# Kernel tuning notes

Hardware: AMD Instinct MI355X
Metric: run time of the kernel (lower is better)

The kernel has to match this reference:

```python
import jax, jax.numpy as jnp
import numpy as np

BETA = 0.25
ALPHA = 0.5
K = 1024
D = 64


def setup_inputs() -> dict:
    key = jax.random.key(0)
    k1, k2 = jax.random.split(key)
    latents = jax.random.normal(k1, (32, D, 64, 64), dtype=jnp.float32)  # NCHW
    # nn.Embedding init uniform_(-1/K, 1/K)
    emb_weight = jax.random.uniform(k2, (K, D), dtype=jnp.float32, minval=-1.0 / K, maxval=1.0 / K)
    return {"latents": latents, "emb_weight": emb_weight}


def reference(latents, emb_weight):
    # NCHW -> NHWC
    x = jnp.transpose(latents, (0, 2, 3, 1))  # [B,H,W,D]
    B, H, W, Dd = x.shape
    flat = x.reshape(-1, Dd)  # [N,D]

    dist = (jnp.sum(flat * flat, axis=1, keepdims=True)
            + jnp.sum(emb_weight * emb_weight, axis=1)
            - 2.0 * flat @ emb_weight.T)
    inds = jnp.argmin(dist, axis=1)  # [N]

    # one-hot @ W == gather
    q = emb_weight[inds].reshape(B, H, W, Dd)

    commitment_loss = jnp.mean((jax.lax.stop_gradient(q) - x) ** 2)
    embedding_loss = jnp.mean((q - jax.lax.stop_gradient(x)) ** 2)
    vq_loss = commitment_loss * BETA + embedding_loss * ALPHA

    alpha_q = 2.0 * ALPHA / (B * H * W * Dd)
    q_st = x + alpha_q * q + jax.lax.stop_gradient((1.0 - alpha_q) * q - x)

    out = jnp.transpose(q_st, (0, 3, 1, 2))  # NHWC -> NCHW
    return out, vq_loss, inds.reshape(B, H, W)
```

## Files before the change

kernel.cpp:

```cpp
#include <hip/hip_runtime.h>

typedef __attribute__((ext_vector_type(8))) short bf16x8;
typedef __attribute__((ext_vector_type(4))) float f32x4;
typedef __attribute__((ext_vector_type(4))) int   i32x4;

#define NROWS     131072
#define KCODES    1024
#define DDIM      64
#define OUT_ELEMS 8388608
#define NBLK      1024
#define MAGICF    12582912.0f
#define MARGIN    240
#define WS_PART   0
#define WS_SE     (8*1024)
#define WS_SEM    (12*1024)
#define WS_BPREP  (16*1024)

__device__ __forceinline__ float pairwise64_sq(const float* __restrict__ v) {
#pragma clang fp contract(off)
    float r[8];
#pragma unroll
    for (int j = 0; j < 8; ++j) r[j] = v[j] * v[j];
#pragma unroll
    for (int i = 8; i < 64; i += 8) {
#pragma unroll
        for (int j = 0; j < 8; ++j) r[j] += v[i + j] * v[i + j];
    }
    return ((r[0] + r[1]) + (r[2] + r[3])) + ((r[4] + r[5]) + (r[6] + r[7]));
}

__device__ __forceinline__ int med3i(int a, int b, int c) {
    int mn = min(a, b), mx = max(a, b);
    return max(mn, min(mx, c));
}

__device__ __forceinline__ unsigned short rne_bf16(float v) {
    unsigned u = __float_as_uint(v);
    return (unsigned short)((u + 0x7fffu + ((u >> 16) & 1u)) >> 16);
}

__global__ __launch_bounds__(256) void vq_prep(
    const float* __restrict__ emb, float* __restrict__ se,
    float* __restrict__ sem, unsigned short* __restrict__ bprep)
{
#pragma clang fp contract(off)
    const int k = blockIdx.x * 256 + threadIdx.x;
    if (k >= KCODES) return;
    const float* e = emb + (k << 6);
    float s = pairwise64_sq(e);
    se[k]  = s;
    sem[k] = (s * 65536.0f) + MAGICF;

    const int c = k >> 4, slot = k & 15;
#pragma unroll
    for (int f = 0; f < 2; ++f) {
#pragma unroll
        for (int g = 0; g < 4; ++g) {
            unsigned short h[8];
#pragma unroll
            for (int j = 0; j < 8; ++j)
                h[j] = rne_bf16(e[f * 32 + g * 8 + j] * 256.0f);
            int4 w;
            w.x = h[0] | (h[1] << 16); w.y = h[2] | (h[3] << 16);
            w.z = h[4] | (h[5] << 16); w.w = h[6] | (h[7] << 16);
            *reinterpret_cast<int4*>(bprep + (((c * 2 + f) * 64 + (g * 16 + slot)) << 3)) = w;
        }
    }
}

__global__ __launch_bounds__(256, 2) void vq_main(
    const float* __restrict__ lat, const float* __restrict__ emb,
    const float* __restrict__ se_g, const float* __restrict__ sem_g,
    const unsigned short* __restrict__ bprep,
    float* __restrict__ out, double* __restrict__ partials)
{
#pragma clang fp contract(off)
    __shared__ float  x_lds[128 * 67];
    __shared__ float  se_lds[KCODES];
    __shared__ float  sem_lds[KCODES];
    __shared__ int    keys_lds[128 * 49];
    __shared__ int    idx_lds[128];
    __shared__ double wsum[4];

    const int tid = threadIdx.x, l = tid & 63, wv = tid >> 6;
    const int blk = blockIdx.x;
    const int n0 = blk * 128, b = n0 >> 12, hw0 = n0 & 4095;

    {
        const int row = tid & 127, dh = (tid >> 7) * 32;
#pragma unroll
        for (int dd = 0; dd < 32; ++dd) {
            int d = dh + dd;
            x_lds[row * 67 + d] = lat[((size_t)b << 18) + ((size_t)d << 12) + hw0 + row];
        }
    }
    for (int i = tid; i < KCODES; i += 256) { se_lds[i] = se_g[i]; sem_lds[i] = sem_g[i]; }
    __syncthreads();

    bf16x8 afrag[2][2];
#pragma unroll
    for (int T = 0; T < 2; ++T) {
        const float* xr = x_lds + (wv * 32 + T * 16 + (l & 15)) * 67;
        const int kb = (l >> 4) << 3;
#pragma unroll
        for (int kh = 0; kh < 2; ++kh) {
            bf16x8 f;
#pragma unroll
            for (int j = 0; j < 8; ++j)
                f[j] = (short)rne_bf16(xr[kh * 32 + kb + j] * -512.0f);
            afrag[T][kh] = f;
        }
    }

    int m1[2][4], m2[2][4], m3[2][4];
#pragma unroll
    for (int T = 0; T < 2; ++T)
#pragma unroll
        for (int r = 0; r < 4; ++r) { m1[T][r] = m2[T][r] = m3[T][r] = 0x7fffffff; }

    const i32x4* bp = reinterpret_cast<const i32x4*>(bprep);
    i32x4 bbuf[2][2];
    bbuf[0][0] = bp[l];
    bbuf[0][1] = bp[64 + l];

#pragma unroll 2
    for (int c = 0; c < 64; ++c) {
        const int cur = c & 1, nxt = cur ^ 1;
        if (c < 63) {
            bbuf[nxt][0] = bp[(c + 1) * 128 + l];
            bbuf[nxt][1] = bp[(c + 1) * 128 + 64 + l];
        }
        const float sevm = sem_lds[c * 16 + (l & 15)];
        bf16x8 b0 = __builtin_bit_cast(bf16x8, bbuf[cur][0]);
        bf16x8 b1 = __builtin_bit_cast(bf16x8, bbuf[cur][1]);
        const unsigned code0 = (unsigned)((c << 4) + (l & 15));
#pragma unroll
        for (int T = 0; T < 2; ++T) {
            f32x4 acc = {0.f, 0.f, 0.f, 0.f};
            acc = __builtin_amdgcn_mfma_f32_16x16x32_bf16(afrag[T][0], b0, acc, 0, 0, 0);
            acc = __builtin_amdgcn_mfma_f32_16x16x32_bf16(afrag[T][1], b1, acc, 0, 0, 0);
#pragma unroll
            for (int r = 0; r < 4; ++r) {
                float uf = acc[r] + sevm;
                int key = (int)((__float_as_uint(uf) << 10) | code0);
                int n1 = min(key, m1[T][r]);
                int n2 = med3i(key, m1[T][r], m2[T][r]);
                int n3 = med3i(max(key, m1[T][r]), m2[T][r], m3[T][r]);
                m1[T][r] = n1; m2[T][r] = n2; m3[T][r] = n3;
            }
        }
    }

#pragma unroll
    for (int T = 0; T < 2; ++T) {
#pragma unroll
        for (int r = 0; r < 4; ++r) {
            const int rloc = wv * 32 + T * 16 + ((l >> 4) << 2) + r;
            keys_lds[rloc * 49 + (l & 15) * 3 + 0] = m1[T][r];
            keys_lds[rloc * 49 + (l & 15) * 3 + 1] = m2[T][r];
            keys_lds[rloc * 49 + (l & 15) * 3 + 2] = m3[T][r];
        }
    }
    __syncthreads();

    if (tid < 128) {
        const int row = tid;
        int mk = 0x7fffffff;
#pragma unroll 4
        for (int i = 0; i < 48; ++i) mk = min(mk, keys_lds[row * 49 + i]);
        const int lim = mk + (MARGIN << 10) + 1023;
        const float* xr = x_lds + row * 67;
        const float sx = pairwise64_sq(xr);
        float bestd = 3.4e38f; int besti = KCODES;
        for (int i = 0; i < 48; ++i) {
            int key = keys_lds[row * 49 + i];
            if (key <= lim) {
                int code = key & 1023;
                const float* e = emb + (code << 6);
                float g = 0.0f;
#pragma unroll
                for (int d = 0; d < 64; ++d) g = fmaf(xr[d], e[d], g);
                float s_   = sx + se_lds[code];
                float dist = s_ - 2.0f * g;
                if (dist < bestd || (dist == bestd && code < besti)) { bestd = dist; besti = code; }
            }
        }
        idx_lds[row] = besti;
    }
    __syncthreads();

    double lsum = 0.0;
    {
        const float aq = 1.0f / 8388608.0f;
        const int row = tid & 127, dh = (tid >> 7) * 32;
        const int code = idx_lds[row];
        float q[32];
        const float4* eq4 = reinterpret_cast<const float4*>(emb + (code << 6) + dh);
#pragma unroll
        for (int qq = 0; qq < 8; ++qq) {
            float4 v = eq4[qq];
            q[qq * 4 + 0] = v.x; q[qq * 4 + 1] = v.y; q[qq * 4 + 2] = v.z; q[qq * 4 + 3] = v.w;
        }
        float* ob = out + ((size_t)b << 18) + hw0 + row;
#pragma unroll
        for (int dd = 0; dd < 32; ++dd) {
            int d = dh + dd;
            float xv = x_lds[row * 67 + d];
            float qd = q[dd];
            float v  = (xv + aq * qd) + ((1.0f - aq) * qd - xv);
            ob[(size_t)d << 12] = v;
            float diff = qd - xv;
            lsum += (double)diff * (double)diff;
        }
    }
    if (tid < 128) out[OUT_ELEMS + 1 + (size_t)n0 + tid] = (float)idx_lds[tid];

#pragma unroll
    for (int off = 32; off > 0; off >>= 1) lsum += __shfl_down(lsum, off, 64);
    if (l == 0) wsum[wv] = lsum;
    __syncthreads();
    if (tid == 0) partials[blk] = (wsum[0] + wsum[1]) + (wsum[2] + wsum[3]);
}

__global__ __launch_bounds__(512) void vq_finish(
    const double* __restrict__ partials, float* __restrict__ out)
{
    __shared__ double lds[8];
    const int t = threadIdx.x;
    double s = partials[t] + partials[t + 512];
#pragma unroll
    for (int off = 32; off > 0; off >>= 1) s += __shfl_down(s, off, 64);
    if ((t & 63) == 0) lds[t >> 6] = s;
    __syncthreads();
    if (t == 0) {
        double tot = 0.0;
#pragma unroll
        for (int i = 0; i < 8; ++i) tot += lds[i];
        out[OUT_ELEMS] = (float)(0.75 * tot / (double)OUT_ELEMS);
    }
}

extern "C" void kernel_launch(void* const* d_in, const int* in_sizes, int n_in,
                              void* d_out, int out_size, void* d_ws, size_t ws_size,
                              hipStream_t stream)
{
    const float* lat = (const float*)d_in[0];
    const float* emb = (const float*)d_in[1];
    float* out = (float*)d_out;
    char* ws = (char*)d_ws;

    double* partials      = (double*)(ws + WS_PART);
    float* se             = (float*)(ws + WS_SE);
    float* sem            = (float*)(ws + WS_SEM);
    unsigned short* bprep = (unsigned short*)(ws + WS_BPREP);

    vq_prep<<<dim3(4),    dim3(256), 0, stream>>>(emb, se, sem, bprep);
    vq_main<<<dim3(NBLK), dim3(256), 0, stream>>>(lat, emb, se, sem, bprep, out, partials);
    vq_finish<<<dim3(1),  dim3(512), 0, stream>>>(partials, out);
}
```

Measured before the change: 97.60 us.

## Halve rows per block and split candidate rescoring across four lanes

Each block now handles 64 rows instead of 128, doubling the grid to 2048 blocks. Each wave now computes one 16-row MFMA tile instead of two. The exact-distance rescoring of the top-3 candidates, previously done serially by 128 threads over 48 keys, is now split across four lanes per row with shuffle reductions. This is meant to raise occupancy and balance the serial refinement phase, at the cost of loading the codebook prefetch and se tables twice as often per row. The change in x-norm summation order may slightly alter tie-breaking numerics.

```diff
diff --git a/kernel.cpp b/kernel.cpp
--- a/kernel.cpp
+++ b/kernel.cpp
@@ -6,15 +6,16 @@
 
 #define NROWS     131072
 #define KCODES    1024
-#define DDIM      64
 #define OUT_ELEMS 8388608
-#define NBLK      1024
+#define RPB       64
+#define NBLK      2048
 #define MAGICF    12582912.0f
 #define MARGIN    240
+#define XSTRIDE   67
 #define WS_PART   0
-#define WS_SE     (8*1024)
-#define WS_SEM    (12*1024)
-#define WS_BPREP  (16*1024)
+#define WS_SE     (16*1024)
+#define WS_SEM    (20*1024)
+#define WS_BPREP  (24*1024)
 
 __device__ __forceinline__ float pairwise64_sq(const float* __restrict__ v) {
 #pragma clang fp contract(off)
@@ -75,48 +76,46 @@
     float* __restrict__ out, double* __restrict__ partials)
 {
 #pragma clang fp contract(off)
-    __shared__ float  x_lds[128 * 67];
+    __shared__ float  x_lds[RPB * XSTRIDE];
     __shared__ float  se_lds[KCODES];
     __shared__ float  sem_lds[KCODES];
-    __shared__ int    keys_lds[128 * 49];
-    __shared__ int    idx_lds[128];
+    __shared__ int    keys_lds[RPB * 49];
+    __shared__ int    idx_lds[RPB];
     __shared__ double wsum[4];
 
     const int tid = threadIdx.x, l = tid & 63, wv = tid >> 6;
     const int blk = blockIdx.x;
-    const int n0 = blk * 128, b = n0 >> 12, hw0 = n0 & 4095;
-
-    {
-        const int row = tid & 127, dh = (tid >> 7) * 32;
-#pragma unroll
-        for (int dd = 0; dd < 32; ++dd) {
-            int d = dh + dd;
-            x_lds[row * 67 + d] = lat[((size_t)b << 18) + ((size_t)d << 12) + hw0 + row];
+    const int n0 = blk * RPB, b = n0 >> 12, hw0 = n0 & 4095;
+    const float* latb = lat + ((size_t)b << 18) + hw0;
+
+    {
+        const int row = tid & 63, dbase = (tid >> 6) * 16;
+#pragma unroll
+        for (int dd = 0; dd < 16; ++dd) {
+            int d = dbase + dd;
+            x_lds[row * XSTRIDE + d] = latb[((size_t)d << 12) + row];
         }
     }
     for (int i = tid; i < KCODES; i += 256) { se_lds[i] = se_g[i]; sem_lds[i] = sem_g[i]; }
     __syncthreads();
 
-    bf16x8 afrag[2][2];
-#pragma unroll
-    for (int T = 0; T < 2; ++T) {
-        const float* xr = x_lds + (wv * 32 + T * 16 + (l & 15)) * 67;
-        const int kb = (l >> 4) << 3;
+    bf16x8 afrag[2];
+    {
+        const int arow = l & 15, kb = (l >> 4) << 3;
+        const float* xr = x_lds + (wv * 16 + arow) * XSTRIDE;
 #pragma unroll
         for (int kh = 0; kh < 2; ++kh) {
             bf16x8 f;
 #pragma unroll
             for (int j = 0; j < 8; ++j)
                 f[j] = (short)rne_bf16(xr[kh * 32 + kb + j] * -512.0f);
-            afrag[T][kh] = f;
-        }
-    }
-
-    int m1[2][4], m2[2][4], m3[2][4];
-#pragma unroll
-    for (int T = 0; T < 2; ++T)
-#pragma unroll
-        for (int r = 0; r < 4; ++r) { m1[T][r] = m2[T][r] = m3[T][r] = 0x7fffffff; }
+            afrag[kh] = f;
+        }
+    }
+
+    int m1[4], m2[4], m3[4];
+#pragma unroll
+    for (int r = 0; r < 4; ++r) { m1[r] = m2[r] = m3[r] = 0x7fffffff; }
 
     const i32x4* bp = reinterpret_cast<const i32x4*>(bprep);
     i32x4 bbuf[2][2];
@@ -134,86 +133,105 @@
         bf16x8 b0 = __builtin_bit_cast(bf16x8, bbuf[cur][0]);
         bf16x8 b1 = __builtin_bit_cast(bf16x8, bbuf[cur][1]);
         const unsigned code0 = (unsigned)((c << 4) + (l & 15));
-#pragma unroll
-        for (int T = 0; T < 2; ++T) {
-            f32x4 acc = {0.f, 0.f, 0.f, 0.f};
-            acc = __builtin_amdgcn_mfma_f32_16x16x32_bf16(afrag[T][0], b0, acc, 0, 0, 0);
-            acc = __builtin_amdgcn_mfma_f32_16x16x32_bf16(afrag[T][1], b1, acc, 0, 0, 0);
-#pragma unroll
-            for (int r = 0; r < 4; ++r) {
-                float uf = acc[r] + sevm;
-                int key = (int)((__float_as_uint(uf) << 10) | code0);
-                int n1 = min(key, m1[T][r]);
-                int n2 = med3i(key, m1[T][r], m2[T][r]);
-                int n3 = med3i(max(key, m1[T][r]), m2[T][r], m3[T][r]);
-                m1[T][r] = n1; m2[T][r] = n2; m3[T][r] = n3;
-            }
-        }
-    }
-
-#pragma unroll
-    for (int T = 0; T < 2; ++T) {
+        f32x4 acc = {0.f, 0.f, 0.f, 0.f};
+        acc = __builtin_amdgcn_mfma_f32_16x16x32_bf16(afrag[0], b0, acc, 0, 0, 0);
+        acc = __builtin_amdgcn_mfma_f32_16x16x32_bf16(afrag[1], b1, acc, 0, 0, 0);
 #pragma unroll
         for (int r = 0; r < 4; ++r) {
-            const int rloc = wv * 32 + T * 16 + ((l >> 4) << 2) + r;
-            keys_lds[rloc * 49 + (l & 15) * 3 + 0] = m1[T][r];
-            keys_lds[rloc * 49 + (l & 15) * 3 + 1] = m2[T][r];
-            keys_lds[rloc * 49 + (l & 15) * 3 + 2] = m3[T][r];
-        }
-    }
-    __syncthreads();
-
-    if (tid < 128) {
-        const int row = tid;
+            float uf = acc[r] + sevm;
+            int key = (int)((__float_as_uint(uf) << 10) | code0);
+            int n1 = min(key, m1[r]);
+            int n2 = med3i(key, m1[r], m2[r]);
+            int n3 = med3i(max(key, m1[r]), m2[r], m3[r]);
+            m1[r] = n1; m2[r] = n2; m3[r] = n3;
+        }
+    }
+
+#pragma unroll
+    for (int r = 0; r < 4; ++r) {
+        const int rloc = wv * 16 + ((l >> 4) << 2) + r;
+        keys_lds[rloc * 49 + (l & 15) * 3 + 0] = m1[r];
+        keys_lds[rloc * 49 + (l & 15) * 3 + 1] = m2[r];
+        keys_lds[rloc * 49 + (l & 15) * 3 + 2] = m3[r];
+    }
+    __syncthreads();
+
+    {
+        const int row = tid >> 2, h = tid & 3;
+        const int kbase = row * 49 + h * 12;
         int mk = 0x7fffffff;
+#pragma unroll
+        for (int i = 0; i < 12; ++i) mk = min(mk, keys_lds[kbase + i]);
+        mk = min(mk, __shfl_xor(mk, 1, 64));
+        mk = min(mk, __shfl_xor(mk, 2, 64));
+        const int lim = mk + (MARGIN << 10) + 1023;
+
+        const float* xr = x_lds + row * XSTRIDE;
+        float rr0 = 0.0f, rr1 = 0.0f;
+#pragma unroll
+        for (int i = 0; i < 64; i += 8) {
+            float v0 = xr[i + 2 * h];
+            float v1 = xr[i + 2 * h + 1];
+            rr0 += v0 * v0;
+            rr1 += v1 * v1;
+        }
+        float s_h = rr0 + rr1;
+        float p   = s_h + __shfl_xor(s_h, 1, 64);
+        float sx  = p + __shfl_xor(p, 2, 64);
+
+        float bestd = 3.4e38f; int besti = KCODES;
 #pragma unroll 4
-        for (int i = 0; i < 48; ++i) mk = min(mk, keys_lds[row * 49 + i]);
-        const int lim = mk + (MARGIN << 10) + 1023;
-        const float* xr = x_lds + row * 67;
-        const float sx = pairwise64_sq(xr);
-        float bestd = 3.4e38f; int besti = KCODES;
-        for (int i = 0; i < 48; ++i) {
-            int key = keys_lds[row * 49 + i];
+        for (int i = 0; i < 12; ++i) {
+            int key = keys_lds[kbase + i];
             if (key <= lim) {
                 int code = key & 1023;
                 const float* e = emb + (code << 6);
                 float g = 0.0f;
 #pragma unroll
-                for (int d = 0; d < 64; ++d) g = fmaf(xr[d], e[d], g);
-                float s_   = sx + se_lds[code];
-                float dist = s_ - 2.0f * g;
+                for (int d = 0; d < 64; ++d)
+                    g = fmaf(xr[d], e[d], g);
+                float ss   = sx + se_lds[code];
+                float dist = ss - 2.0f * g;
                 if (dist < bestd || (dist == bestd && code < besti)) { bestd = dist; besti = code; }
             }
         }
-        idx_lds[row] = besti;
+#pragma unroll
+        for (int off = 1; off <= 2; off <<= 1) {
+            float od = __shfl_xor(bestd, off, 64);
+            int   oi = __shfl_xor(besti, off, 64);
+            if (od < bestd || (od == bestd && oi < besti)) { bestd = od; besti = oi; }
+        }
+        if (h == 0) {
+            idx_lds[row] = besti;
+            out[OUT_ELEMS + 1 + (size_t)n0 + row] = (float)besti;
+        }
     }
     __syncthreads();
 
     double lsum = 0.0;
     {
         const float aq = 1.0f / 8388608.0f;
-        const int row = tid & 127, dh = (tid >> 7) * 32;
+        const int row = tid & 63, dh = (tid >> 6) * 16;
         const int code = idx_lds[row];
-        float q[32];
         const float4* eq4 = reinterpret_cast<const float4*>(emb + (code << 6) + dh);
-#pragma unroll
-        for (int qq = 0; qq < 8; ++qq) {
-            float4 v = eq4[qq];
-            q[qq * 4 + 0] = v.x; q[qq * 4 + 1] = v.y; q[qq * 4 + 2] = v.z; q[qq * 4 + 3] = v.w;
-        }
+        const float* xr = x_lds + row * XSTRIDE;
         float* ob = out + ((size_t)b << 18) + hw0 + row;
 #pragma unroll
-        for (int dd = 0; dd < 32; ++dd) {
-            int d = dh + dd;
-            float xv = x_lds[row * 67 + d];
-            float qd = q[dd];
-            float v  = (xv + aq * qd) + ((1.0f - aq) * qd - xv);
-            ob[(size_t)d << 12] = v;
-            float diff = qd - xv;
-            lsum += (double)diff * (double)diff;
-        }
-    }
-    if (tid < 128) out[OUT_ELEMS + 1 + (size_t)n0 + tid] = (float)idx_lds[tid];
+        for (int qq = 0; qq < 4; ++qq) {
+            float4 qv = eq4[qq];
+            float qa[4] = {qv.x, qv.y, qv.z, qv.w};
+#pragma unroll
+            for (int u = 0; u < 4; ++u) {
+                int d = dh + qq * 4 + u;
+                float xv = xr[d];
+                float qd = qa[u];
+                float v  = (xv + aq * qd) + ((1.0f - aq) * qd - xv);
+                ob[(size_t)d << 12] = v;
+                float diff = qd - xv;
+                lsum += (double)diff * (double)diff;
+            }
+        }
+    }
 
 #pragma unroll
     for (int off = 32; off > 0; off >>= 1) lsum += __shfl_down(lsum, off, 64);
@@ -227,7 +245,7 @@
 {
     __shared__ double lds[8];
     const int t = threadIdx.x;
-    double s = partials[t] + partials[t + 512];
+    double s = ((partials[t] + partials[t + 512]) + partials[t + 1024]) + partials[t + 1536];
 #pragma unroll
     for (int off = 32; off > 0; off >>= 1) s += __shfl_down(s, off, 64);
     if ((t & 63) == 0) lds[t >> 6] = s;
```

Result: no change. 97.02 us (-0.6%).
